# Kernel tuning notes

Hardware: AMD Instinct MI355X
Metric: run time of the kernel (lower is better)

Reference implementation:

```python
import jax, jax.numpy as jnp
import numpy as np

B, IN, H, F, T = 4096, 1024, 1024, 128, 3
LN_EPS = 1e-5


def setup_inputs() -> dict:
    key = jax.random.key(0)
    ks = jax.random.split(key, 12)
    inp = {
        "input_": jax.random.normal(ks[0], (B, IN), jnp.float32),
        "hx": jax.random.normal(ks[1], (B, H), jnp.float32),
        "cx": jax.random.normal(ks[2], (B, H), jnp.float32),
        "topic_w": jax.random.uniform(ks[3], (B, T), jnp.float32),
        # factorized gate weights (init scales per reset_parameters)
        "w_ih_a": jax.random.normal(ks[4], (4 * H, F), jnp.float32) / jnp.sqrt(F),
        "w_ih_b": jnp.full((F, T), 0.1 / T, jnp.float32),
        "w_ih_c": jax.random.normal(ks[5], (F, IN), jnp.float32) / jnp.sqrt(IN),
        "w_hh_a": 0.1 * jax.random.normal(ks[6], (4 * H, F), jnp.float32),
        "w_hh_b": jnp.full((F, T), 0.1 / T, jnp.float32),
        "w_hh_c": 0.1 * jax.random.normal(ks[7], (F, H), jnp.float32),
        # theta transforms: weight=0, bias=1 per reset_parameters
        "th_ih_w": jnp.zeros((T, T), jnp.float32),
        "th_ih_b": jnp.ones((T,), jnp.float32),
        "th_hh_w": jnp.zeros((T, T), jnp.float32),
        "th_hh_b": jnp.ones((T,), jnp.float32),
        # layernorm params
        "ln_i_w": jnp.ones((4 * H,), jnp.float32),
        "ln_i_b": jnp.zeros((4 * H,), jnp.float32),
        "ln_h_w": jnp.ones((4 * H,), jnp.float32),
        "ln_h_b": jnp.zeros((4 * H,), jnp.float32),
        "ln_c_w": jnp.ones((H,), jnp.float32),
        "ln_c_b": jnp.zeros((H,), jnp.float32),
    }
    return inp


def _ln(x, w, b):
    mu = x.mean(-1, keepdims=True)
    var = ((x - mu) ** 2).mean(-1, keepdims=True)
    return (x - mu) * jax.lax.rsqrt(var + LN_EPS) * w + b


def reference(input_, hx, cx, topic_w,
              w_ih_a, w_ih_b, w_ih_c, w_hh_a, w_hh_b, w_hh_c,
              th_ih_w, th_ih_b, th_hh_w, th_hh_b,
              ln_i_w, ln_i_b, ln_h_w, ln_h_b, ln_c_w, ln_c_b):
    # factorized input gates: ((x @ C^T) * (theta(topic) @ B^T)) @ A^T
    scale_i = (topic_w @ th_ih_w.T + th_ih_b) @ w_ih_b.T            # [B, F]
    igates = ((input_ @ w_ih_c.T) * scale_i) @ w_ih_a.T             # [B, 4H]
    scale_h = (topic_w @ th_hh_w.T + th_hh_b) @ w_hh_b.T            # [B, F]
    hgates = ((hx @ w_hh_c.T) * scale_h) @ w_hh_a.T                 # [B, 4H]

    gates = _ln(igates, ln_i_w, ln_i_b) + _ln(hgates, ln_h_w, ln_h_b)
    i, f, g, o = jnp.split(gates, 4, axis=1)
    i = jax.nn.sigmoid(i)
    f = jax.nn.sigmoid(f)
    g = jnp.tanh(g)  # dropout p=0 -> identity
    o = jax.nn.sigmoid(o)
    cy = _ln(f * cx + i * g, ln_c_w, ln_c_b)
    hy = o * jnp.tanh(cy)
    return hy, cy
```

## Files before the change

kernel.cpp:

```cpp
#include <hip/hip_runtime.h>

typedef unsigned short ushort_t;
typedef __attribute__((ext_vector_type(8))) short bf8_t;
typedef __attribute__((ext_vector_type(4))) float f4_t;

#define B_   4096
#define IN_  1024
#define H_   1024
#define F_   128
#define G4_  4096
#define EPS_ 1e-5f

#define NG1   512
#define NPREP 256
#define NGRAM 128

__device__ __forceinline__ float us2f(unsigned short s) {
  union { unsigned int u; float f; } v;
  v.u = ((unsigned int)s) << 16;
  return v.f;
}
__device__ __forceinline__ unsigned short f2us(float f) {
  union { float f; unsigned int u; } v;
  v.f = f;
  unsigned int r = (v.u + 0x7fffu + ((v.u >> 16) & 1u)) >> 16;
  return (unsigned short)r;
}
__device__ __forceinline__ float sigf(float x) { return 1.0f / (1.0f + __expf(-x)); }
__device__ __forceinline__ float tanh_f(float x) { return 1.0f - 2.0f / (1.0f + __expf(2.0f * x)); }

__device__ __forceinline__ int detect_fp32(const void* disc) {
  return ((const unsigned int*)disc)[0] == 0x3F800000u;
}
__device__ __forceinline__ float ldf(const void* p, int i, int fp32) {
  return fp32 ? ((const float*)p)[i] : us2f(((const ushort_t*)p)[i]);
}
__device__ __forceinline__ void ld8(const void* p, int idx, float* o, int fp32) {
  if (fp32) {
    const float4* q = (const float4*)((const float*)p + idx);
    float4 v0 = q[0], v1 = q[1];
    o[0]=v0.x; o[1]=v0.y; o[2]=v0.z; o[3]=v0.w;
    o[4]=v1.x; o[5]=v1.y; o[6]=v1.z; o[7]=v1.w;
  } else {
    uint4 v = *(const uint4*)((const ushort_t*)p + idx);
    const ushort_t* pv = (const ushort_t*)&v;
    #pragma unroll
    for (int i = 0; i < 8; i++) o[i] = us2f(pv[i]);
  }
}
__device__ __forceinline__ bf8_t cvt8p(const float* f) {
  union { bf8_t v; unsigned int u[4]; } r;
  const unsigned int* ui = (const unsigned int*)f;
  #pragma unroll
  for (int i = 0; i < 4; i++) {
    unsigned int lo = ui[2 * i] + 0x8000u;
    unsigned int hi = ui[2 * i + 1] + 0x8000u;
    r.u[i] = __builtin_amdgcn_perm(hi, lo, 0x07060302u);
  }
  return r.v;
}

__global__ __launch_bounds__(256, 4) void k_stageA(
    const void* __restrict__ X0, const void* __restrict__ X1,
    const void* __restrict__ Wc0, const void* __restrict__ Wc1,
    const void* __restrict__ topic,
    const void* __restrict__ thw0, const void* __restrict__ thw1,
    const void* __restrict__ thb0, const void* __restrict__ thb1,
    const void* __restrict__ wsb0, const void* __restrict__ wsb1,
    const void* __restrict__ Ai, const void* __restrict__ Ah,
    const void* __restrict__ lnwi, const void* __restrict__ lnwh,
    ushort_t* __restrict__ wb,
    float* __restrict__ cm_i, float* __restrict__ cm_h,
    float* __restrict__ g_i, float* __restrict__ g_h,
    float* __restrict__ C0, float* __restrict__ C1)
{
  __shared__ float smem[32 * 128];
  int bid = blockIdx.x, tid = threadIdx.x;
  int fp32 = detect_fp32(lnwi);

  if (bid < NG1) {
    int rb = bid >> 1, mat = bid & 1;
    const void* X   = mat ? X1 : X0;
    const void* W   = mat ? Wc1 : Wc0;
    const void* thw = mat ? thw1 : thw0;
    const void* thb = mat ? thb1 : thb0;
    const void* wbp = mat ? wsb1 : wsb0;
    float* C = mat ? C1 : C0;
    int lane = tid & 63, w = tid >> 6;
    int quad = lane >> 4, lcol = lane & 15;
    int brow0 = rb * 16;

    f4_t acc[2];
    acc[0] = (f4_t){0.f, 0.f, 0.f, 0.f};
    acc[1] = (f4_t){0.f, 0.f, 0.f, 0.f};

    #pragma unroll 4
    for (int kc = 0; kc < 32; kc++) {
      int kb = kc * 32 + quad * 8;
      float a[8];
      ld8(X, (brow0 + lcol) * IN_ + kb, a, fp32);
      bf8_t af = cvt8p(a);
      #pragma unroll
      for (int t = 0; t < 2; t++) {
        float bt[8];
        ld8(W, ((w * 2 + t) * 16 + lcol) * IN_ + kb, bt, fp32);
        acc[t] = __builtin_amdgcn_mfma_f32_16x16x32_bf16(af, cvt8p(bt), acc[t], 0, 0, 0);
      }
    }

    float thwf[3][3], thbf[3];
    #pragma unroll
    for (int t = 0; t < 3; t++) {
      thbf[t] = ldf(thb, t, fp32);
      #pragma unroll
      for (int t2 = 0; t2 < 3; t2++) thwf[t][t2] = ldf(thw, t * 3 + t2, fp32);
    }
    float tmpv[4][3];
    #pragma unroll
    for (int reg = 0; reg < 4; reg++) {
      int b = brow0 + quad * 4 + reg;
      float tp0 = ldf(topic, b * 3 + 0, fp32);
      float tp1 = ldf(topic, b * 3 + 1, fp32);
      float tp2 = ldf(topic, b * 3 + 2, fp32);
      #pragma unroll
      for (int t = 0; t < 3; t++)
        tmpv[reg][t] = thbf[t] + tp0 * thwf[t][0] + tp1 * thwf[t][1] + tp2 * thwf[t][2];
    }
    #pragma unroll
    for (int t = 0; t < 2; t++) {
      int f = (w * 2 + t) * 16 + lcol;
      float wv0 = ldf(wbp, f * 3 + 0, fp32);
      float wv1 = ldf(wbp, f * 3 + 1, fp32);
      float wv2 = ldf(wbp, f * 3 + 2, fp32);
      #pragma unroll
      for (int reg = 0; reg < 4; reg++) {
        float sc = tmpv[reg][0] * wv0 + tmpv[reg][1] * wv1 + tmpv[reg][2] * wv2;
        C[(brow0 + quad * 4 + reg) * F_ + f] = acc[t][reg] * sc;
      }
    }
  } else if (bid < NG1 + NPREP) {
    int t = bid - NG1;
    #pragma unroll
    for (int i = 0; i < 16; i++) {
      int e = i * 256 + tid;
      int c = e >> 9, l = (e >> 3) & 63, j = e & 7;
      int k = c * 32 + ((l >> 4) << 3) + j;
      int n = t * 16 + (l & 15);
      float v;
      if (k < 128) v = ldf(Ai, n * F_ + k, fp32) * ldf(lnwi, n, fp32);
      else         v = ldf(Ah, n * F_ + (k - 128), fp32) * ldf(lnwh, n, fp32);
      wb[(size_t)t * 4096 + e] = f2us(v);
    }
    const void* A = (tid < 128) ? Ai : Ah;
    float* cm = (tid < 128) ? cm_i : cm_h;
    int f = tid & 127;
    float s = 0.f;
    #pragma unroll
    for (int i = 0; i < 16; i++) s += ldf(A, (t * 16 + i) * F_ + f, fp32);
    atomicAdd(&cm[f], s);
  } else {
    int g = bid - (NG1 + NPREP);
    int fblk = g & 3, mat = (g >> 2) & 1, z = g >> 3;
    const void* A = mat ? Ah : Ai;
    float* G = mat ? g_h : g_i;
    float (*As)[128] = (float(*)[128])smem;
    int f1_0 = fblk * 32;
    int tf2 = tid & 31, tf1 = tid >> 5;
    float acc[4][4] = {};
    int nbase = z * 256;
    for (int n0 = nbase; n0 < nbase + 256; n0 += 32) {
      #pragma unroll
      for (int j = 0; j < 2; j++) {
        int idx = tid + 256 * j;
        int nn = idx >> 4, f8 = (idx & 15) * 8;
        float t[8];
        ld8(A, (n0 + nn) * F_ + f8, t, fp32);
        #pragma unroll
        for (int i = 0; i < 8; i++) As[nn][f8 + i] = t[i];
      }
      __syncthreads();
      #pragma unroll 4
      for (int nn = 0; nn < 32; nn++) {
        float4 a1 = *(const float4*)&As[nn][f1_0 + 4 * tf1];
        float4 a2 = *(const float4*)&As[nn][4 * tf2];
        const float* x1 = (const float*)&a1;
        const float* x2 = (const float*)&a2;
        #pragma unroll
        for (int i = 0; i < 4; i++)
          #pragma unroll
          for (int j = 0; j < 4; j++) acc[i][j] += x1[i] * x2[j];
      }
      __syncthreads();
    }
    #pragma unroll
    for (int i = 0; i < 4; i++)
      #pragma unroll
      for (int j = 0; j < 4; j++)
        atomicAdd(&G[(f1_0 + 4 * tf1 + i) * F_ + 4 * tf2 + j], acc[i][j]);
  }
}

__global__ __launch_bounds__(256, 4) void k_stats2(
    const float* __restrict__ C0, const float* __restrict__ C1,
    const float* __restrict__ g_i, const float* __restrict__ g_h,
    const float* __restrict__ cm_i, const float* __restrict__ cm_h,
    float* __restrict__ mrs_i, float* __restrict__ mrs_h,
    ushort_t* __restrict__ xb)
{
  int bid = blockIdx.x;
  int rb = bid >> 1, mat = bid & 1;
  const float* C  = mat ? C1 : C0;
  const float* G  = mat ? g_h : g_i;
  const float* cm = mat ? cm_h : cm_i;
  float* mrs = mat ? mrs_h : mrs_i;
  int kbase = mat ? 128 : 0;

  int tid = threadIdx.x;
  int lane = tid & 63, w = tid >> 6;
  int quad = lane >> 4, lcol = lane & 15;
  int b0 = rb * 16;

  __shared__ float p1part[4][16];
  __shared__ float p2s[16];
  __shared__ float rs_s[16];

  bf8_t af[4];
  float p2p = 0.f;
  #pragma unroll
  for (int kc = 0; kc < 4; kc++) {
    int kb = kc * 32 + quad * 8;
    const float4* q = (const float4*)(C + (b0 + lcol) * F_ + kb);
    float4 v0 = q[0], v1 = q[1];
    float a[8] = {v0.x, v0.y, v0.z, v0.w, v1.x, v1.y, v1.z, v1.w};
    af[kc] = cvt8p(a);
    if (w == 0) {
      #pragma unroll
      for (int j = 0; j < 8; j++) p2p += a[j] * cm[kb + j];
    }
  }

  float p1p[4] = {0.f, 0.f, 0.f, 0.f};
  #pragma unroll
  for (int t = 0; t < 2; t++) {
    int colf = (w * 2 + t) * 16 + lcol;
    f4_t acc = {0.f, 0.f, 0.f, 0.f};
    #pragma unroll
    for (int kc = 0; kc < 4; kc++) {
      const float4* qg = (const float4*)(G + colf * F_ + kc * 32 + quad * 8);
      float4 w0 = qg[0], w1 = qg[1];
      float bt[8] = {w0.x, w0.y, w0.z, w0.w, w1.x, w1.y, w1.z, w1.w};
      acc = __builtin_amdgcn_mfma_f32_16x16x32_bf16(af[kc], cvt8p(bt), acc, 0, 0, 0);
    }
    #pragma unroll
    for (int reg = 0; reg < 4; reg++)
      p1p[reg] += acc[reg] * C[(b0 + quad * 4 + reg) * F_ + colf];
  }
  #pragma unroll
  for (int d = 1; d < 16; d <<= 1)
    #pragma unroll
    for (int reg = 0; reg < 4; reg++)
      p1p[reg] += __shfl_xor(p1p[reg], d, 64);
  if (lcol == 0) {
    #pragma unroll
    for (int reg = 0; reg < 4; reg++)
      p1part[w][quad * 4 + reg] = p1p[reg];
  }
  if (w == 0) {
    p2p += __shfl_xor(p2p, 16, 64);
    p2p += __shfl_xor(p2p, 32, 64);
    if (quad == 0) p2s[lcol] = p2p;
  }
  __syncthreads();
  if (tid < 16) {
    float p1 = p1part[0][tid] + p1part[1][tid] + p1part[2][tid] + p1part[3][tid];
    float E2 = p1 * (1.0f / 4096.0f);
    float mu = p2s[tid] * (1.0f / 4096.0f);
    float var = E2 - mu * mu;
    float rs = rsqrtf(var + EPS_);
    rs_s[tid] = rs;
    mrs[b0 + tid] = mu * rs;
  }
  __syncthreads();
  int f = tid & 127, half = tid >> 7;
  ushort_t* xbb = xb + (size_t)rb * 4096;
  int k = kbase + f;
  int c = k >> 5, lq = (k >> 3) & 3, j = k & 7;
  #pragma unroll
  for (int i = 0; i < 8; i++) {
    int r2 = half * 8 + i;
    int lfrag = r2 | (lq << 4);
    xbb[c * 512 + lfrag * 8 + j] = f2us(C[(b0 + r2) * F_ + f] * rs_s[r2]);
  }
}

__global__ __launch_bounds__(1024, 4) void k_fused(
    const ushort_t* __restrict__ xb, const ushort_t* __restrict__ wb,
    const float* __restrict__ mrs_i, const float* __restrict__ mrs_h,
    const void* __restrict__ lniw, const void* __restrict__ lnib,
    const void* __restrict__ lnhw, const void* __restrict__ lnhb,
    const void* __restrict__ lncw, const void* __restrict__ lncb,
    const void* __restrict__ cx, float* __restrict__ out)
{
  __shared__ float buf[16][1028];
  __shared__ float obuf[16][1028];
  __shared__ float wpart[16][16][2];
  __shared__ float mu_s[16], rs_s[16];
  int tid = threadIdx.x;
  int lane = tid & 63, w = tid >> 6;
  int quad = lane >> 4, lcol = lane & 15;
  int b0 = blockIdx.x * 16;
  int fp32 = detect_fp32(lniw);

  #pragma unroll
  for (int pass = 0; pass < 2; pass++) {
    int e = pass * 8192 + tid * 8;
    int r = e >> 10, c = e & 1023;
    float t[8];
    ld8(cx, (b0 + r) * H_ + c, t, fp32);
    *(float4*)&buf[r][c] = *(float4*)&t[0];
    *(float4*)&buf[r][c + 4] = *(float4*)&t[4];
  }

  const ushort_t* xblk = xb + (size_t)blockIdx.x * 4096;

  float mi[4], mh[4];
  #pragma unroll
  for (int reg = 0; reg < 4; reg++) {
    mi[reg] = mrs_i[b0 + quad * 4 + reg];
    mh[reg] = mrs_h[b0 + quad * 4 + reg];
  }
  __syncthreads();

  float s1[4] = {0.f, 0.f, 0.f, 0.f}, s2[4] = {0.f, 0.f, 0.f, 0.f};

  #pragma unroll
  for (int q = 0; q < 4; q++) {
    int cg = w * 4 + q;
    int col = cg * 16 + lcol;
    bf8_t af[8];
    #pragma unroll
    for (int c = 0; c < 8; c++)
      af[c] = *(const bf8_t*)(xblk + c * 512 + lane * 8);
    f4_t accg[4];
    #pragma unroll
    for (int g = 0; g < 4; g++) {
      f4_t acc = {0.f, 0.f, 0.f, 0.f};
      int t = g * 64 + cg;
      const ushort_t* wt = wb + (size_t)t * 4096 + lane * 8;
      #pragma unroll
      for (int c = 0; c < 8; c++) {
        bf8_t bf = *(const bf8_t*)(wt + c * 512);
        acc = __builtin_amdgcn_mfma_f32_16x16x32_bf16(af[c], bf, acc, 0, 0, 0);
      }
      accg[g] = acc;
    }
    float liw0 = ldf(lniw, 0 * H_ + col, fp32), lib0 = ldf(lnib, 0 * H_ + col, fp32);
    float lhw0 = ldf(lnhw, 0 * H_ + col, fp32), lhb0 = ldf(lnhb, 0 * H_ + col, fp32);
    float liw1 = ldf(lniw, 1 * H_ + col, fp32), lib1 = ldf(lnib, 1 * H_ + col, fp32);
    float lhw1 = ldf(lnhw, 1 * H_ + col, fp32), lhb1 = ldf(lnhb, 1 * H_ + col, fp32);
    float liw2 = ldf(lniw, 2 * H_ + col, fp32), lib2 = ldf(lnib, 2 * H_ + col, fp32);
    float lhw2 = ldf(lnhw, 2 * H_ + col, fp32), lhb2 = ldf(lnhb, 2 * H_ + col, fp32);
    float liw3 = ldf(lniw, 3 * H_ + col, fp32), lib3 = ldf(lnib, 3 * H_ + col, fp32);
    float lhw3 = ldf(lnhw, 3 * H_ + col, fp32), lhb3 = ldf(lnhb, 3 * H_ + col, fp32);
    #pragma unroll
    for (int reg = 0; reg < 4; reg++) {
      int m = quad * 4 + reg;
      float gi = accg[0][reg] + lib0 + lhb0 - mi[reg] * liw0 - mh[reg] * lhw0;
      float gf = accg[1][reg] + lib1 + lhb1 - mi[reg] * liw1 - mh[reg] * lhw1;
      float gg = accg[2][reg] + lib2 + lhb2 - mi[reg] * liw2 - mh[reg] * lhw2;
      float go = accg[3][reg] + lib3 + lhb3 - mi[reg] * liw3 - mh[reg] * lhw3;
      float iv = sigf(gi), fv = sigf(gf), gv = tanh_f(gg), ov = sigf(go);
      float cxv = buf[m][col];
      float cval = fv * cxv + iv * gv;
      buf[m][col] = cval;
      obuf[m][col] = ov;
      s1[reg] += cval;
      s2[reg] += cval * cval;
    }
  }

  #pragma unroll
  for (int d = 1; d < 16; d <<= 1) {
    #pragma unroll
    for (int reg = 0; reg < 4; reg++) {
      s1[reg] += __shfl_xor(s1[reg], d, 64);
      s2[reg] += __shfl_xor(s2[reg], d, 64);
    }
  }
  if (lcol == 0) {
    #pragma unroll
    for (int reg = 0; reg < 4; reg++) {
      wpart[w][quad * 4 + reg][0] = s1[reg];
      wpart[w][quad * 4 + reg][1] = s2[reg];
    }
  }
  __syncthreads();
  if (tid < 16) {
    float t1 = 0.f, t2 = 0.f;
    #pragma unroll
    for (int ww = 0; ww < 16; ww++) { t1 += wpart[ww][tid][0]; t2 += wpart[ww][tid][1]; }
    float mu = t1 * (1.0f / 1024.0f);
    float var = t2 * (1.0f / 1024.0f) - mu * mu;
    mu_s[tid] = mu;
    rs_s[tid] = rsqrtf(var + EPS_);
  }
  __syncthreads();

  #pragma unroll
  for (int q = 0; q < 4; q++) {
    int col = (w * 4 + q) * 16 + lcol;
    float lw = ldf(lncw, col, fp32), lb = ldf(lncb, col, fp32);
    #pragma unroll
    for (int reg = 0; reg < 4; reg++) {
      int m = quad * 4 + reg;
      float cyv = (buf[m][col] - mu_s[m]) * rs_s[m] * lw + lb;
      buf[m][col] = cyv;
      obuf[m][col] = obuf[m][col] * tanh_f(cyv);
    }
  }
  __syncthreads();
  #pragma unroll
  for (int pass = 0; pass < 2; pass++) {
    int e = pass * 8192 + tid * 8;
    int r = e >> 10, c = e & 1023;
    float4 c0 = *(const float4*)&buf[r][c];
    float4 c1v = *(const float4*)&buf[r][c + 4];
    *(float4*)&out[(size_t)B_ * H_ + (b0 + r) * H_ + c] = c0;
    *(float4*)&out[(size_t)B_ * H_ + (b0 + r) * H_ + c + 4] = c1v;
    float4 h0 = *(const float4*)&obuf[r][c];
    float4 h1 = *(const float4*)&obuf[r][c + 4];
    *(float4*)&out[(b0 + r) * H_ + c] = h0;
    *(float4*)&out[(b0 + r) * H_ + c + 4] = h1;
  }
}

extern "C" void kernel_launch(void* const* d_in, const int* in_sizes, int n_in,
                              void* d_out, int out_size, void* d_ws, size_t ws_size,
                              hipStream_t stream) {
  const void* input_  = d_in[0];
  const void* hx      = d_in[1];
  const void* cx      = d_in[2];
  const void* topic   = d_in[3];
  const void* w_ih_a  = d_in[4];
  const void* w_ih_b  = d_in[5];
  const void* w_ih_c  = d_in[6];
  const void* w_hh_a  = d_in[7];
  const void* w_hh_b  = d_in[8];
  const void* w_hh_c  = d_in[9];
  const void* th_ih_w = d_in[10];
  const void* th_ih_b = d_in[11];
  const void* th_hh_w = d_in[12];
  const void* th_hh_b = d_in[13];
  const void* ln_i_w  = d_in[14];
  const void* ln_i_b  = d_in[15];
  const void* ln_h_w  = d_in[16];
  const void* ln_h_b  = d_in[17];
  const void* ln_c_w  = d_in[18];
  const void* ln_c_b  = d_in[19];

  float* w = (float*)d_ws;
  float* c1    = w;
  float* c2    = c1 + B_ * F_;
  float* g_i   = c2 + B_ * F_;
  float* g_h   = g_i + F_ * F_;
  float* cm_i  = g_h + F_ * F_;
  float* cm_h  = cm_i + F_;
  float* mrs_i = cm_h + F_;
  float* mrs_h = mrs_i + B_;
  ushort_t* xb = (ushort_t*)(mrs_h + B_);
  ushort_t* wbf = xb + (size_t)B_ * 256;

  hipMemsetAsync(g_i, 0, (size_t)(2 * F_ * F_ + 2 * F_) * sizeof(float), stream);

  k_stageA<<<dim3(NG1 + NPREP + NGRAM), dim3(256), 0, stream>>>(
      input_, hx, w_ih_c, w_hh_c, topic,
      th_ih_w, th_hh_w, th_ih_b, th_hh_b, w_ih_b, w_hh_b,
      w_ih_a, w_hh_a, ln_i_w, ln_h_w,
      wbf, cm_i, cm_h, g_i, g_h, c1, c2);
  k_stats2<<<dim3(512), dim3(256), 0, stream>>>(
      c1, c2, g_i, g_h, cm_i, cm_h, mrs_i, mrs_h, xb);
  k_fused<<<dim3(256), dim3(1024), 0, stream>>>(
      xb, wbf, mrs_i, mrs_h,
      ln_i_w, ln_i_b, ln_h_w, ln_h_b, ln_c_w, ln_c_b, cx, (float*)d_out);
}
```

Measured before the change: 235.2 us.

## Stage x fragment in LDS, load cx directly, write outputs without LDS staging

The fused kernel now copies the block's bf16 x fragment into shared memory once and reads it per k-chunk. It interleaves the four gate MFMAs per chunk instead of running four sequential chains. cx is loaded straight from global memory into registers rather than staged through LDS, and hy/cy are written directly from the normalization loop, dropping the final LDS round trip and a barrier. The cost is scalar, 16-column-strided global stores and loads in place of wide float4 transfers, and launch_bounds no longer requests 4 blocks per CU.

Result: faster. 226.3 us (-3.8%).

```diff
diff --git a/kernel.cpp b/kernel.cpp
--- a/kernel.cpp
+++ b/kernel.cpp
@@ -293,7 +293,7 @@
   }
 }
 
-__global__ __launch_bounds__(1024, 4) void k_fused(
+__global__ __launch_bounds__(1024) void k_fused(
     const ushort_t* __restrict__ xb, const ushort_t* __restrict__ wb,
     const float* __restrict__ mrs_i, const float* __restrict__ mrs_h,
     const void* __restrict__ lniw, const void* __restrict__ lnib,
@@ -303,6 +303,7 @@
 {
   __shared__ float buf[16][1028];
   __shared__ float obuf[16][1028];
+  __shared__ ushort_t xs[4096];
   __shared__ float wpart[16][16][2];
   __shared__ float mu_s[16], rs_s[16];
   int tid = threadIdx.x;
@@ -311,17 +312,8 @@
   int b0 = blockIdx.x * 16;
   int fp32 = detect_fp32(lniw);
 
-  #pragma unroll
-  for (int pass = 0; pass < 2; pass++) {
-    int e = pass * 8192 + tid * 8;
-    int r = e >> 10, c = e & 1023;
-    float t[8];
-    ld8(cx, (b0 + r) * H_ + c, t, fp32);
-    *(float4*)&buf[r][c] = *(float4*)&t[0];
-    *(float4*)&buf[r][c + 4] = *(float4*)&t[4];
-  }
-
-  const ushort_t* xblk = xb + (size_t)blockIdx.x * 4096;
+  ((unsigned long long*)xs)[tid] =
+      ((const unsigned long long*)(xb + (size_t)blockIdx.x * 4096))[tid];
 
   float mi[4], mh[4];
   #pragma unroll
@@ -337,22 +329,22 @@
   for (int q = 0; q < 4; q++) {
     int cg = w * 4 + q;
     int col = cg * 16 + lcol;
-    bf8_t af[8];
-    #pragma unroll
-    for (int c = 0; c < 8; c++)
-      af[c] = *(const bf8_t*)(xblk + c * 512 + lane * 8);
+    float cxv[4];
+    #pragma unroll
+    for (int reg = 0; reg < 4; reg++)
+      cxv[reg] = ldf(cx, (size_t)(b0 + quad * 4 + reg) * H_ + col, fp32);
+
     f4_t accg[4];
     #pragma unroll
-    for (int g = 0; g < 4; g++) {
-      f4_t acc = {0.f, 0.f, 0.f, 0.f};
-      int t = g * 64 + cg;
-      const ushort_t* wt = wb + (size_t)t * 4096 + lane * 8;
-      #pragma unroll
-      for (int c = 0; c < 8; c++) {
-        bf8_t bf = *(const bf8_t*)(wt + c * 512);
-        acc = __builtin_amdgcn_mfma_f32_16x16x32_bf16(af[c], bf, acc, 0, 0, 0);
+    for (int g = 0; g < 4; g++) accg[g] = (f4_t){0.f, 0.f, 0.f, 0.f};
+    #pragma unroll
+    for (int c = 0; c < 8; c++) {
+      bf8_t af = *(const bf8_t*)&xs[c * 512 + lane * 8];
+      #pragma unroll
+      for (int g = 0; g < 4; g++) {
+        bf8_t bf = *(const bf8_t*)(wb + (size_t)(g * 64 + cg) * 4096 + c * 512 + lane * 8);
+        accg[g] = __builtin_amdgcn_mfma_f32_16x16x32_bf16(af, bf, accg[g], 0, 0, 0);
       }
-      accg[g] = acc;
     }
     float liw0 = ldf(lniw, 0 * H_ + col, fp32), lib0 = ldf(lnib, 0 * H_ + col, fp32);
     float lhw0 = ldf(lnhw, 0 * H_ + col, fp32), lhb0 = ldf(lnhb, 0 * H_ + col, fp32);
@@ -370,8 +362,7 @@
       float gg = accg[2][reg] + lib2 + lhb2 - mi[reg] * liw2 - mh[reg] * lhw2;
       float go = accg[3][reg] + lib3 + lhb3 - mi[reg] * liw3 - mh[reg] * lhw3;
       float iv = sigf(gi), fv = sigf(gf), gv = tanh_f(gg), ov = sigf(go);
-      float cxv = buf[m][col];
-      float cval = fv * cxv + iv * gv;
+      float cval = fv * cxv[reg] + iv * gv;
       buf[m][col] = cval;
       obuf[m][col] = ov;
       s1[reg] += cval;
@@ -414,23 +405,9 @@
     for (int reg = 0; reg < 4; reg++) {
       int m = quad * 4 + reg;
       float cyv = (buf[m][col] - mu_s[m]) * rs_s[m] * lw + lb;
-      buf[m][col] = cyv;
-      obuf[m][col] = obuf[m][col] * tanh_f(cyv);
-    }
-  }
-  __syncthreads();
-  #pragma unroll
-  for (int pass = 0; pass < 2; pass++) {
-    int e = pass * 8192 + tid * 8;
-    int r = e >> 10, c = e & 1023;
-    float4 c0 = *(const float4*)&buf[r][c];
-    float4 c1v = *(const float4*)&buf[r][c + 4];
-    *(float4*)&out[(size_t)B_ * H_ + (b0 + r) * H_ + c] = c0;
-    *(float4*)&out[(size_t)B_ * H_ + (b0 + r) * H_ + c + 4] = c1v;
-    float4 h0 = *(const float4*)&obuf[r][c];
-    float4 h1 = *(const float4*)&obuf[r][c + 4];
-    *(float4*)&out[(b0 + r) * H_ + c] = h0;
-    *(float4*)&out[(b0 + r) * H_ + c + 4] = h1;
+      out[(size_t)B_ * H_ + (size_t)(b0 + m) * H_ + col] = cyv;
+      out[(size_t)(b0 + m) * H_ + col] = obuf[m][col] * tanh_f(cyv);
+    }
   }
 }
 
```
